# Kernel tuning notes

Hardware: AMD Instinct MI355X
Metric: run time of the kernel (lower is better)

## Reference

```python
import jax, jax.numpy as jnp
import numpy as np

# Static config matching init_kwargs
DG = 8          # deformable groups
KH, KW = 3, 3
STRIDE, PAD, DIL = 1, 1, 1


def setup_inputs() -> dict:
    key = jax.random.key(0)
    k1, k2, k3, k4 = jax.random.split(key, 4)
    B, C, H, W = 4, 128, 128, 128
    Cout = 128
    K = KH * KW
    x = jax.random.normal(k1, (B, C, H, W), dtype=jnp.float32)
    offset = jax.random.normal(k2, (B, 2 * DG * K, H, W), dtype=jnp.float32)
    mask = jax.random.uniform(k3, (B, DG * K, H, W), dtype=jnp.float32)
    stdv = 1.0 / np.sqrt(C * KH * KW)
    weight = jax.random.uniform(k4, (Cout, C, KH, KW), dtype=jnp.float32,
                                minval=-stdv, maxval=stdv)
    bias = jnp.zeros((Cout,), dtype=jnp.float32)
    return {"x": x, "offset": offset, "mask": mask, "weight": weight, "bias": bias}


def _deform_conv2d(x, offset, mask, weight, bias):
    B, C, H, W = x.shape
    Cout = weight.shape[0]
    K = KH * KW
    Ho = (H + 2 * PAD - DIL * (KH - 1) - 1) // STRIDE + 1
    Wo = (W + 2 * PAD - DIL * (KW - 1) - 1) // STRIDE + 1
    Cg = C // DG

    # offsets: channel layout [dg, k, (dy, dx)]
    off = offset.reshape(B, DG, K, 2, Ho, Wo)
    dy, dx = off[:, :, :, 0], off[:, :, :, 1]          # [B, DG, K, Ho, Wo]
    m = mask.reshape(B, DG, K, Ho, Wo)

    ky, kx = jnp.meshgrid(jnp.arange(KH), jnp.arange(KW), indexing='ij')
    ky, kx = ky.reshape(K), kx.reshape(K)
    # base sampling grid per kernel tap: [K, Ho] / [K, Wo]
    py = (jnp.arange(Ho) * STRIDE - PAD)[None, :] + (ky * DIL)[:, None]
    px = (jnp.arange(Wo) * STRIDE - PAD)[None, :] + (kx * DIL)[:, None]

    sy = dy + py[None, None, :, :, None].astype(dy.dtype)  # [B, DG, K, Ho, Wo]
    sx = dx + px[None, None, :, None, :].astype(dx.dtype)

    y0f = jnp.floor(sy); x0f = jnp.floor(sx)
    ly = sy - y0f; lx = sx - x0f
    y0 = y0f.astype(jnp.int32); x0 = x0f.astype(jnp.int32)

    x_g = x.reshape(B, DG, Cg, H * W)

    def gather(iy, ix):
        valid = ((iy >= 0) & (iy < H) & (ix >= 0) & (ix < W)).astype(x.dtype)
        idx = jnp.clip(iy, 0, H - 1) * W + jnp.clip(ix, 0, W - 1)
        flat = idx.reshape(B, DG, 1, K * Ho * Wo)
        v = jnp.take_along_axis(x_g, flat, axis=3).reshape(B, DG, Cg, K, Ho, Wo)
        return v * valid[:, :, None]

    w00 = ((1 - ly) * (1 - lx))[:, :, None]
    w01 = ((1 - ly) * lx)[:, :, None]
    w10 = (ly * (1 - lx))[:, :, None]
    w11 = (ly * lx)[:, :, None]

    val = (gather(y0, x0) * w00 + gather(y0, x0 + 1) * w01 +
           gather(y0 + 1, x0) * w10 + gather(y0 + 1, x0 + 1) * w11)
    val = val * m[:, :, None]                         # modulation
    sampled = val.reshape(B, C, K, Ho, Wo)

    w = weight.reshape(Cout, C, K)
    out = jnp.einsum('bckhw,ock->bohw', sampled, w)
    return out + bias[None, :, None, None]


def reference(x, offset, mask, weight, bias):
    return _deform_conv2d(x, offset, mask, weight, bias)
```

## Files before the change

kernel.cpp:

```cpp
#include <hip/hip_runtime.h>
#include <hip/hip_fp16.h>


#define NB    4
#define NC    128
#define NH    128
#define NW    128
#define NCOUT 128
#define NDG   8
#define NCG   16
#define NK    9
#define NCK   1152
#define NHW   16384
#define TP    64
#define BKC   288
#define ROWP  296

typedef __attribute__((ext_vector_type(4))) float f32x4;
typedef _Float16 half8 __attribute__((ext_vector_type(8)));

union C16 { uint4 u[2]; __half2 h[8]; };

__global__ __launch_bounds__(256)
void prep(const float* __restrict__ x, const float* __restrict__ w,
          ushort* __restrict__ xt, ushort* __restrict__ wf) {
  __shared__ __align__(16) unsigned LDSU[1024 * 9];
  const int tid = threadIdx.x;

  if (blockIdx.x < 128) {
    const int o = blockIdx.x;
    float* WL = (float*)LDSU;
    const float4* src = (const float4*)(w + o * NCK);
    for (int i = tid; i < NCK / 4; i += 256) ((float4*)WL)[i] = src[i];
    __syncthreads();
    unsigned* dst = (unsigned*)wf + o * (NCK / 2);
    for (int t = tid; t < NCK / 2; t += 256) {
      const int g = t / 72, r2 = t - g * 72;
      const int k = r2 >> 3, cg2 = r2 & 7;
      const int c = g * NCG + cg2 * 2;
      const unsigned h0 = __half_as_ushort(__float2half_rn(WL[c * NK + k]));
      const unsigned h1 = __half_as_ushort(__float2half_rn(WL[(c + 1) * NK + k]));
      dst[t] = h0 | (h1 << 16);
    }
  } else {
    const int blk  = blockIdx.x - 128;
    const int slab = blk >> 4;
    const int hw0  = (blk & 15) * 1024;
    const float* xb = x + (size_t)slab * NCG * NHW + hw0;
#pragma unroll
    for (int cp = 0; cp < 8; ++cp) {
#pragma unroll
      for (int i = 0; i < 4; ++i) {
        const int hw = tid + 256 * i;
        const float f0 = xb[(2 * cp) * NHW + hw];
        const float f1 = xb[(2 * cp + 1) * NHW + hw];
        const unsigned h0 = __half_as_ushort(__float2half_rn(f0));
        const unsigned h1 = __half_as_ushort(__float2half_rn(f1));
        LDSU[hw * 9 + cp] = h0 | (h1 << 16);
      }
    }
    __syncthreads();
    uint4* dst = (uint4*)(xt + ((size_t)slab * NHW + hw0) * NCG);
#pragma unroll
    for (int j = 0; j < 8; ++j) {
      const int lin = tid + 256 * j;
      const int hw = lin >> 1, q = lin & 1;
      uint4 v;
      v.x = LDSU[hw * 9 + q * 4 + 0];
      v.y = LDSU[hw * 9 + q * 4 + 1];
      v.z = LDSU[hw * 9 + q * 4 + 2];
      v.w = LDSU[hw * 9 + q * 4 + 3];
      dst[lin] = v;
    }
  }
}

__global__ __launch_bounds__(256, 4)
void dcn_main(const float* __restrict__ off,
              const float* __restrict__ msk,
              const ushort* __restrict__ xt,
              const ushort* __restrict__ wt,
              const float* __restrict__ bias,
              float* __restrict__ out) {
  __shared__ __align__(16) ushort S[TP * ROWP];

  const int tid  = threadIdx.x;
  const int pos0 = blockIdx.x * TP;
  const int b    = pos0 >> 14;
  const int ho   = (pos0 >> 7) & 127;
  const int wo0  = pos0 & 127;

  const int lane = tid & 63;
  const int wv   = tid >> 6;
  const int l15  = lane & 15;
  const int kq   = lane >> 4;

  const float* offB = off + (size_t)b * 144 * NHW + ho * NW + wo0;
  const float* mskB = msk + (size_t)b * 72  * NHW + ho * NW + wo0;

  f32x4 acc[4][2];
#pragma unroll
  for (int m = 0; m < 4; ++m) {
    acc[m][0] = {0.f, 0.f, 0.f, 0.f};
    acc[m][1] = {0.f, 0.f, 0.f, 0.f};
  }

  for (int ch = 0; ch < 4; ++ch) {
    if (ch) __syncthreads();

#pragma unroll
    for (int it = 0; it < 5; ++it) {
      const int t = tid + it * 256;
      if (t < TP * 18) {
        const int p  = t & 63;
        const int j  = t >> 6;
        const int gl = j / 9;
        const int k  = j - gl * 9;
        const int g  = ch * 2 + gl;
        const int gk = g * 9 + k;
        const int ky = k / 3, kx = k - ky * 3;
        const int wo = wo0 + p;

        const float dy = offB[(gk * 2) * NHW + p];
        const float dx = offB[(gk * 2 + 1) * NHW + p];
        const float mm = mskB[gk * NHW + p];

        const float sy = dy + (float)(ho - 1 + ky);
        const float sx = dx + (float)(wo - 1 + kx);
        const float y0f = floorf(sy), x0f = floorf(sx);
        const float ly = sy - y0f, lx = sx - x0f;
        const int y0 = (int)y0f, x0 = (int)x0f;
        const int y1 = y0 + 1,  x1 = x0 + 1;
        const float hy = 1.f - ly, hx = 1.f - lx;

        float w00 = hy * hx * mm, w01 = hy * lx * mm;
        float w10 = ly * hx * mm, w11 = ly * lx * mm;
        if (y0 < 0 || y0 >= NH) { w00 = 0.f; w01 = 0.f; }
        if (y1 < 0 || y1 >= NH) { w10 = 0.f; w11 = 0.f; }
        if (x0 < 0 || x0 >= NW) { w00 = 0.f; w10 = 0.f; }
        if (x1 < 0 || x1 >= NW) { w01 = 0.f; w11 = 0.f; }

        const int yc0 = min(max(y0, 0), NH - 1);
        const int yc1 = min(max(y1, 0), NH - 1);
        const int xc0 = min(max(x0, 0), NW - 1);
        const int xc1 = min(max(x1, 0), NW - 1);

        const ushort* xg = xt + (size_t)(b * NDG + g) * NHW * NCG;
        const uint4* q00 = (const uint4*)(xg + (yc0 * NW + xc0) * NCG);
        const uint4* q01 = (const uint4*)(xg + (yc0 * NW + xc1) * NCG);
        const uint4* q10 = (const uint4*)(xg + (yc1 * NW + xc0) * NCG);
        const uint4* q11 = (const uint4*)(xg + (yc1 * NW + xc1) * NCG);

        C16 v00, v01, v10, v11, r;
        v00.u[0] = q00[0]; v00.u[1] = q00[1];
        v01.u[0] = q01[0]; v01.u[1] = q01[1];
        v10.u[0] = q10[0]; v10.u[1] = q10[1];
        v11.u[0] = q11[0]; v11.u[1] = q11[1];

        const __half2 W00 = __float2half2_rn(w00);
        const __half2 W01 = __float2half2_rn(w01);
        const __half2 W10 = __float2half2_rn(w10);
        const __half2 W11 = __float2half2_rn(w11);
#pragma unroll
        for (int i = 0; i < 8; ++i) {
          __half2 a = __hmul2(v00.h[i], W00);
          a = __hfma2(v01.h[i], W01, a);
          a = __hfma2(v10.h[i], W10, a);
          a = __hfma2(v11.h[i], W11, a);
          r.h[i] = a;
        }
        ushort* dp = &S[p * ROWP + j * 16];
        *(uint4*)dp = r.u[0];
        *((uint4*)dp + 1) = r.u[1];
      }
    }
    __syncthreads();

    const ushort* bw0 = wt + (size_t)(wv * 32 + l15) * NCK + ch * BKC + kq * 8;
    const ushort* bw1 = bw0 + 16 * NCK;
    const ushort* sa  = &S[l15 * ROWP + kq * 8];
#pragma unroll 3
    for (int kk = 0; kk < BKC; kk += 32) {
      const half8 b0 = *(const half8*)(bw0 + kk);
      const half8 b1 = *(const half8*)(bw1 + kk);
#pragma unroll
      for (int m = 0; m < 4; ++m) {
        const half8 a = *(const half8*)(sa + m * 16 * ROWP + kk);
        acc[m][0] = __builtin_amdgcn_mfma_f32_16x16x32_f16(a, b0, acc[m][0], 0, 0, 0);
        acc[m][1] = __builtin_amdgcn_mfma_f32_16x16x32_f16(a, b1, acc[m][1], 0, 0, 0);
      }
    }
  }

#pragma unroll
  for (int n = 0; n < 2; ++n) {
    const int c0 = wv * 32 + n * 16 + l15;
    const float bs = bias[c0];
    float* op = out + (size_t)(b * NCOUT + c0) * NHW + ho * NW + wo0 + kq * 4;
#pragma unroll
    for (int m = 0; m < 4; ++m) {
      float4 r = {acc[m][n][0] + bs, acc[m][n][1] + bs,
                  acc[m][n][2] + bs, acc[m][n][3] + bs};
      *(float4*)(op + m * 16) = r;
    }
  }
}

extern "C" void kernel_launch(void* const* d_in, const int* in_sizes, int n_in,
                              void* d_out, int out_size, void* d_ws, size_t ws_size,
                              hipStream_t stream) {
  const float* x    = (const float*)d_in[0];
  const float* off  = (const float*)d_in[1];
  const float* msk  = (const float*)d_in[2];
  const float* wgt  = (const float*)d_in[3];
  const float* bias = (const float*)d_in[4];
  float* out = (float*)d_out;

  ushort* xt = (ushort*)d_ws;
  ushort* wf = xt + (size_t)NB * NDG * NHW * NCG;

  hipLaunchKernelGGL(prep, dim3(640), dim3(256), 0, stream, x, wgt, xt, wf);
  hipLaunchKernelGGL(dcn_main, dim3((NB * NH * NW) / TP), dim3(256), 0, stream,
                     off, msk, xt, wf, bias, out);
}
```

Before: 204.0 us.

## Retile deform conv to full-row blocks with per-group K chunks and padded weights

The main kernel now handles a full output row of 128 positions per 512-thread block (512 blocks) instead of 64-position tiles. The reduction is split into 8 per-group chunks padded from 144 to 160 K elements. Weights are pre-padded with zeros, and the LDS pad columns are zeroed once. Each wave computes 16 output channels by 128 positions with 8 accumulators, so each weight fragment is reused across more positions. This costs more sync phases (8 instead of 4), about 11% wasted MFMA work on padding, uneven sampling load (only 128 threads take a third sample), and fewer blocks, which leaves less parallelism to hide latency.

```diff
diff --git a/kernel.cpp b/kernel.cpp
--- a/kernel.cpp
+++ b/kernel.cpp
@@ -12,14 +12,19 @@
 #define NK    9
 #define NCK   1152
 #define NHW   16384
-#define TP    64
-#define BKC   288
-#define ROWP  296
+#define GK    160
+#define ROWP  168
+#define WROW  1280
 
 typedef __attribute__((ext_vector_type(4))) float f32x4;
 typedef _Float16 half8 __attribute__((ext_vector_type(8)));
 
 union C16 { uint4 u[2]; __half2 h[8]; };
+
+__device__ __forceinline__ unsigned pk2h(float a, float b) {
+  return (unsigned)__half_as_ushort(__float2half_rn(a)) |
+         ((unsigned)__half_as_ushort(__float2half_rn(b)) << 16);
+}
 
 __global__ __launch_bounds__(256)
 void prep(const float* __restrict__ x, const float* __restrict__ w,
@@ -33,14 +38,16 @@
     const float4* src = (const float4*)(w + o * NCK);
     for (int i = tid; i < NCK / 4; i += 256) ((float4*)WL)[i] = src[i];
     __syncthreads();
-    unsigned* dst = (unsigned*)wf + o * (NCK / 2);
-    for (int t = tid; t < NCK / 2; t += 256) {
-      const int g = t / 72, r2 = t - g * 72;
-      const int k = r2 >> 3, cg2 = r2 & 7;
-      const int c = g * NCG + cg2 * 2;
-      const unsigned h0 = __half_as_ushort(__float2half_rn(WL[c * NK + k]));
-      const unsigned h1 = __half_as_ushort(__float2half_rn(WL[(c + 1) * NK + k]));
-      dst[t] = h0 | (h1 << 16);
+    unsigned* dst = (unsigned*)wf + o * (WROW / 2);
+    for (int t = tid; t < WROW / 2; t += 256) {
+      const int g = t / 80, r = t - g * 80;
+      unsigned v = 0;
+      if (r < 72) {
+        const int k = r >> 3;
+        const int c = g * NCG + (r & 7) * 2;
+        v = pk2h(WL[c * NK + k], WL[(c + 1) * NK + k]);
+      }
+      dst[t] = v;
     }
   } else {
     const int blk  = blockIdx.x - 128;
@@ -52,11 +59,8 @@
 #pragma unroll
       for (int i = 0; i < 4; ++i) {
         const int hw = tid + 256 * i;
-        const float f0 = xb[(2 * cp) * NHW + hw];
-        const float f1 = xb[(2 * cp + 1) * NHW + hw];
-        const unsigned h0 = __half_as_ushort(__float2half_rn(f0));
-        const unsigned h1 = __half_as_ushort(__float2half_rn(f1));
-        LDSU[hw * 9 + cp] = h0 | (h1 << 16);
+        LDSU[hw * 9 + cp] =
+            pk2h(xb[(2 * cp) * NHW + hw], xb[(2 * cp + 1) * NHW + hw]);
       }
     }
     __syncthreads();
@@ -75,134 +79,141 @@
   }
 }
 
-__global__ __launch_bounds__(256, 4)
+__device__ __forceinline__ void sample_one(
+    int t, int g, int b, int ho, float dy, float dx, float mm,
+    const ushort* __restrict__ xt, ushort* __restrict__ S) {
+  const int p  = t & 127;
+  const int k  = t >> 7;
+  const int ky = k / 3, kx = k - ky * 3;
+
+  const float sy = dy + (float)(ho - 1 + ky);
+  const float sx = dx + (float)(p - 1 + kx);
+  const float y0f = floorf(sy), x0f = floorf(sx);
+  const float ly = sy - y0f, lx = sx - x0f;
+  const int y0 = (int)y0f, x0 = (int)x0f;
+  const int y1 = y0 + 1,  x1 = x0 + 1;
+  const float hy = 1.f - ly, hx = 1.f - lx;
+
+  float w00 = hy * hx * mm, w01 = hy * lx * mm;
+  float w10 = ly * hx * mm, w11 = ly * lx * mm;
+  if (y0 < 0 || y0 >= NH) { w00 = 0.f; w01 = 0.f; }
+  if (y1 < 0 || y1 >= NH) { w10 = 0.f; w11 = 0.f; }
+  if (x0 < 0 || x0 >= NW) { w00 = 0.f; w10 = 0.f; }
+  if (x1 < 0 || x1 >= NW) { w01 = 0.f; w11 = 0.f; }
+
+  const int yc0 = min(max(y0, 0), NH - 1);
+  const int yc1 = min(max(y1, 0), NH - 1);
+  const int xc0 = min(max(x0, 0), NW - 1);
+  const int xc1 = min(max(x1, 0), NW - 1);
+
+  const ushort* xg = xt + (size_t)(b * NDG + g) * NHW * NCG;
+  const uint4* q00 = (const uint4*)(xg + (yc0 * NW + xc0) * NCG);
+  const uint4* q01 = (const uint4*)(xg + (yc0 * NW + xc1) * NCG);
+  const uint4* q10 = (const uint4*)(xg + (yc1 * NW + xc0) * NCG);
+  const uint4* q11 = (const uint4*)(xg + (yc1 * NW + xc1) * NCG);
+
+  C16 v00, v01, v10, v11, r;
+  v00.u[0] = q00[0]; v00.u[1] = q00[1];
+  v01.u[0] = q01[0]; v01.u[1] = q01[1];
+  v10.u[0] = q10[0]; v10.u[1] = q10[1];
+  v11.u[0] = q11[0]; v11.u[1] = q11[1];
+
+  const __half2 W00 = __float2half2_rn(w00);
+  const __half2 W01 = __float2half2_rn(w01);
+  const __half2 W10 = __float2half2_rn(w10);
+  const __half2 W11 = __float2half2_rn(w11);
+#pragma unroll
+  for (int i = 0; i < 8; ++i) {
+    __half2 a = __hmul2(v00.h[i], W00);
+    a = __hfma2(v01.h[i], W01, a);
+    a = __hfma2(v10.h[i], W10, a);
+    a = __hfma2(v11.h[i], W11, a);
+    r.h[i] = a;
+  }
+  ushort* dp = &S[p * ROWP + k * 16];
+  *(uint4*)dp = r.u[0];
+  *((uint4*)dp + 1) = r.u[1];
+}
+
+__global__ __launch_bounds__(512, 4)
 void dcn_main(const float* __restrict__ off,
               const float* __restrict__ msk,
               const ushort* __restrict__ xt,
-              const ushort* __restrict__ wt,
+              const ushort* __restrict__ wf,
               const float* __restrict__ bias,
               float* __restrict__ out) {
-  __shared__ __align__(16) ushort S[TP * ROWP];
-
-  const int tid  = threadIdx.x;
-  const int pos0 = blockIdx.x * TP;
-  const int b    = pos0 >> 14;
-  const int ho   = (pos0 >> 7) & 127;
-  const int wo0  = pos0 & 127;
+  __shared__ __align__(16) ushort S[128 * ROWP];
+
+  const int tid = threadIdx.x;
+  const int blk = blockIdx.x;
+  const int b   = blk >> 7;
+  const int ho  = blk & 127;
 
   const int lane = tid & 63;
   const int wv   = tid >> 6;
   const int l15  = lane & 15;
   const int kq   = lane >> 4;
 
-  const float* offB = off + (size_t)b * 144 * NHW + ho * NW + wo0;
-  const float* mskB = msk + (size_t)b * 72  * NHW + ho * NW + wo0;
-
-  f32x4 acc[4][2];
-#pragma unroll
-  for (int m = 0; m < 4; ++m) {
-    acc[m][0] = {0.f, 0.f, 0.f, 0.f};
-    acc[m][1] = {0.f, 0.f, 0.f, 0.f};
-  }
-
-  for (int ch = 0; ch < 4; ++ch) {
-    if (ch) __syncthreads();
-
-#pragma unroll
-    for (int it = 0; it < 5; ++it) {
-      const int t = tid + it * 256;
-      if (t < TP * 18) {
-        const int p  = t & 63;
-        const int j  = t >> 6;
-        const int gl = j / 9;
-        const int k  = j - gl * 9;
-        const int g  = ch * 2 + gl;
-        const int gk = g * 9 + k;
-        const int ky = k / 3, kx = k - ky * 3;
-        const int wo = wo0 + p;
-
-        const float dy = offB[(gk * 2) * NHW + p];
-        const float dx = offB[(gk * 2 + 1) * NHW + p];
-        const float mm = mskB[gk * NHW + p];
-
-        const float sy = dy + (float)(ho - 1 + ky);
-        const float sx = dx + (float)(wo - 1 + kx);
-        const float y0f = floorf(sy), x0f = floorf(sx);
-        const float ly = sy - y0f, lx = sx - x0f;
-        const int y0 = (int)y0f, x0 = (int)x0f;
-        const int y1 = y0 + 1,  x1 = x0 + 1;
-        const float hy = 1.f - ly, hx = 1.f - lx;
-
-        float w00 = hy * hx * mm, w01 = hy * lx * mm;
-        float w10 = ly * hx * mm, w11 = ly * lx * mm;
-        if (y0 < 0 || y0 >= NH) { w00 = 0.f; w01 = 0.f; }
-        if (y1 < 0 || y1 >= NH) { w10 = 0.f; w11 = 0.f; }
-        if (x0 < 0 || x0 >= NW) { w00 = 0.f; w10 = 0.f; }
-        if (x1 < 0 || x1 >= NW) { w01 = 0.f; w11 = 0.f; }
-
-        const int yc0 = min(max(y0, 0), NH - 1);
-        const int yc1 = min(max(y1, 0), NH - 1);
-        const int xc0 = min(max(x0, 0), NW - 1);
-        const int xc1 = min(max(x1, 0), NW - 1);
-
-        const ushort* xg = xt + (size_t)(b * NDG + g) * NHW * NCG;
-        const uint4* q00 = (const uint4*)(xg + (yc0 * NW + xc0) * NCG);
-        const uint4* q01 = (const uint4*)(xg + (yc0 * NW + xc1) * NCG);
-        const uint4* q10 = (const uint4*)(xg + (yc1 * NW + xc0) * NCG);
-        const uint4* q11 = (const uint4*)(xg + (yc1 * NW + xc1) * NCG);
-
-        C16 v00, v01, v10, v11, r;
-        v00.u[0] = q00[0]; v00.u[1] = q00[1];
-        v01.u[0] = q01[0]; v01.u[1] = q01[1];
-        v10.u[0] = q10[0]; v10.u[1] = q10[1];
-        v11.u[0] = q11[0]; v11.u[1] = q11[1];
-
-        const __half2 W00 = __float2half2_rn(w00);
-        const __half2 W01 = __float2half2_rn(w01);
-        const __half2 W10 = __float2half2_rn(w10);
-        const __half2 W11 = __float2half2_rn(w11);
-#pragma unroll
-        for (int i = 0; i < 8; ++i) {
-          __half2 a = __hmul2(v00.h[i], W00);
-          a = __hfma2(v01.h[i], W01, a);
-          a = __hfma2(v10.h[i], W10, a);
-          a = __hfma2(v11.h[i], W11, a);
-          r.h[i] = a;
-        }
-        ushort* dp = &S[p * ROWP + j * 16];
-        *(uint4*)dp = r.u[0];
-        *((uint4*)dp + 1) = r.u[1];
+  const float* offB = off + (size_t)b * 144 * NHW + ho * NW;
+  const float* mskB = msk + (size_t)b * 72  * NHW + ho * NW;
+
+  for (int i = tid; i < 128 * 8; i += 512) {
+    ((unsigned*)S)[(i >> 3) * (ROWP / 2) + 72 + (i & 7)] = 0;
+  }
+  __syncthreads();
+
+  f32x4 acc[8];
+#pragma unroll
+  for (int m = 0; m < 8; ++m) acc[m] = {0.f, 0.f, 0.f, 0.f};
+
+  const int t0 = tid;
+  const int t1 = tid + 512;
+  const int t2 = tid + 1024;
+  const int p0 = t0 & 127, k0 = t0 >> 7;
+  const int p1 = t1 & 127, k1 = t1 >> 7;
+  const int p2 = t2 & 127, k2 = t2 >> 7;
+
+  for (int g = 0; g < 8; ++g) {
+    if (g) __syncthreads();
+
+    const int gk0 = g * 9 + k0, gk1 = g * 9 + k1, gk2 = g * 9 + k2;
+    const float dy0 = offB[(gk0 * 2) * NHW + p0];
+    const float dx0 = offB[(gk0 * 2 + 1) * NHW + p0];
+    const float m0  = mskB[gk0 * NHW + p0];
+    const float dy1 = offB[(gk1 * 2) * NHW + p1];
+    const float dx1 = offB[(gk1 * 2 + 1) * NHW + p1];
+    const float m1  = mskB[gk1 * NHW + p1];
+    float dy2 = 0.f, dx2 = 0.f, m2 = 0.f;
+    if (tid < 128) {
+      dy2 = offB[(gk2 * 2) * NHW + p2];
+      dx2 = offB[(gk2 * 2 + 1) * NHW + p2];
+      m2  = mskB[gk2 * NHW + p2];
+    }
+    sample_one(t0, g, b, ho, dy0, dx0, m0, xt, S);
+    sample_one(t1, g, b, ho, dy1, dx1, m1, xt, S);
+    if (tid < 128) sample_one(t2, g, b, ho, dy2, dx2, m2, xt, S);
+    __syncthreads();
+
+    const ushort* bw = wf + (size_t)(wv * 16 + l15) * WROW + g * GK + kq * 8;
+    const ushort* sa = &S[l15 * ROWP + kq * 8];
+#pragma unroll
+    for (int ks = 0; ks < 5; ++ks) {
+      const half8 bfrag = *(const half8*)(bw + ks * 32);
+#pragma unroll
+      for (int m = 0; m < 8; ++m) {
+        const half8 a = *(const half8*)(sa + m * 16 * ROWP + ks * 32);
+        acc[m] = __builtin_amdgcn_mfma_f32_16x16x32_f16(a, bfrag, acc[m], 0, 0, 0);
       }
     }
-    __syncthreads();
-
-    const ushort* bw0 = wt + (size_t)(wv * 32 + l15) * NCK + ch * BKC + kq * 8;
-    const ushort* bw1 = bw0 + 16 * NCK;
-    const ushort* sa  = &S[l15 * ROWP + kq * 8];
-#pragma unroll 3
-    for (int kk = 0; kk < BKC; kk += 32) {
-      const half8 b0 = *(const half8*)(bw0 + kk);
-      const half8 b1 = *(const half8*)(bw1 + kk);
-#pragma unroll
-      for (int m = 0; m < 4; ++m) {
-        const half8 a = *(const half8*)(sa + m * 16 * ROWP + kk);
-        acc[m][0] = __builtin_amdgcn_mfma_f32_16x16x32_f16(a, b0, acc[m][0], 0, 0, 0);
-        acc[m][1] = __builtin_amdgcn_mfma_f32_16x16x32_f16(a, b1, acc[m][1], 0, 0, 0);
-      }
-    }
-  }
-
-#pragma unroll
-  for (int n = 0; n < 2; ++n) {
-    const int c0 = wv * 32 + n * 16 + l15;
-    const float bs = bias[c0];
-    float* op = out + (size_t)(b * NCOUT + c0) * NHW + ho * NW + wo0 + kq * 4;
-#pragma unroll
-    for (int m = 0; m < 4; ++m) {
-      float4 r = {acc[m][n][0] + bs, acc[m][n][1] + bs,
-                  acc[m][n][2] + bs, acc[m][n][3] + bs};
-      *(float4*)(op + m * 16) = r;
-    }
+  }
+
+  const int c0 = wv * 16 + l15;
+  const float bs = bias[c0];
+  float* op = out + (size_t)(b * NCOUT + c0) * NHW + ho * NW + kq * 4;
+#pragma unroll
+  for (int m = 0; m < 8; ++m) {
+    float4 r = {acc[m][0] + bs, acc[m][1] + bs, acc[m][2] + bs, acc[m][3] + bs};
+    *(float4*)(op + m * 16) = r;
   }
 }
 
@@ -220,6 +231,6 @@
   ushort* wf = xt + (size_t)NB * NDG * NHW * NCG;
 
   hipLaunchKernelGGL(prep, dim3(640), dim3(256), 0, stream, x, wgt, xt, wf);
-  hipLaunchKernelGGL(dcn_main, dim3((NB * NH * NW) / TP), dim3(256), 0, stream,
+  hipLaunchKernelGGL(dcn_main, dim3(512), dim3(512), 0, stream,
                      off, msk, xt, wf, bias, out);
 }
```

New measurement: 188.4 us. -7.6%, faster.
